# Performance work log

Measured on AMD Instinct MI355X. Metric: run time of the kernel, lower is better.

Reference implementation:

```python
import jax, jax.numpy as jnp
import numpy as np

COST_BBOX = 5.0
COST_GIOU = 2.0


def box_cxcywh_to_xyxy(b):
    cx, cy, w, h = b[:, 0], b[:, 1], b[:, 2], b[:, 3]
    return jnp.stack([cx - 0.5 * w, cy - 0.5 * h, cx + 0.5 * w, cy + 0.5 * h], axis=-1)


def generalized_box_iou(boxes1, boxes2):
    # boxes1 [N,4], boxes2 [M,4] in xyxy -> [N,M] GIoU
    area1 = (boxes1[:, 2] - boxes1[:, 0]) * (boxes1[:, 3] - boxes1[:, 1])
    area2 = (boxes2[:, 2] - boxes2[:, 0]) * (boxes2[:, 3] - boxes2[:, 1])
    lt = jnp.maximum(boxes1[:, None, :2], boxes2[None, :, :2])
    rb = jnp.minimum(boxes1[:, None, 2:], boxes2[None, :, 2:])
    wh = jnp.clip(rb - lt, 0.0)
    inter = wh[..., 0] * wh[..., 1]
    union = area1[:, None] + area2[None, :] - inter
    iou = inter / union
    lt_e = jnp.minimum(boxes1[:, None, :2], boxes2[None, :, :2])
    rb_e = jnp.maximum(boxes1[:, None, 2:], boxes2[None, :, 2:])
    wh_e = jnp.clip(rb_e - lt_e, 0.0)
    area_e = wh_e[..., 0] * wh_e[..., 1]
    return iou - (area_e - union) / area_e


@jax.jit
def cost_matrix(pred_boxes, truth_boxes):
    B, Q, _ = pred_boxes.shape
    out_bbox = pred_boxes.reshape(-1, 4)   # [B*Q,4]
    tgt_bbox = truth_boxes.reshape(-1, 4)  # [B*T,4]
    cost_bbox = jnp.sum(jnp.abs(out_bbox[:, None, :] - tgt_bbox[None, :, :]), axis=-1)  # L1 cdist
    cost_giou = -generalized_box_iou(box_cxcywh_to_xyxy(out_bbox), box_cxcywh_to_xyxy(tgt_bbox))
    C = COST_BBOX * cost_bbox + COST_GIOU * cost_giou
    return C.reshape(B, Q, -1)


def _lsa_rows_le_cols(cost):
    # Jonker-Volgenant shortest augmenting path (same algorithm as scipy
    # linear_sum_assignment). cost: [R, C] float64 with R <= C.
    # Returns col4row: assigned column for each row.
    R, Cc = cost.shape
    u = np.zeros(R)
    v = np.zeros(Cc)
    col4row = np.full(R, -1, dtype=np.int64)
    row4col = np.full(Cc, -1, dtype=np.int64)
    for cur in range(R):
        shortest = np.full(Cc, np.inf)
        path = np.full(Cc, -1, dtype=np.int64)
        on_row = np.zeros(R, dtype=bool)
        on_col = np.zeros(Cc, dtype=bool)
        min_val = 0.0
        i = cur
        sink = -1
        while sink == -1:
            on_row[i] = True
            rem = np.where(~on_col)[0]
            d = min_val + cost[i, rem] - u[i] - v[rem]
            better = d < shortest[rem]
            upd = rem[better]
            shortest[upd] = d[better]
            path[upd] = i
            j = rem[np.argmin(shortest[rem])]
            min_val = shortest[j]
            on_col[j] = True
            if row4col[j] == -1:
                sink = j
            else:
                i = row4col[j]
        u[cur] += min_val
        rset = np.where(on_row)[0]
        rset = rset[rset != cur]
        u[rset] += min_val - shortest[col4row[rset]]
        cset = np.where(on_col)[0]
        v[cset] -= min_val - shortest[cset]
        # augment along the path back from sink
        j = sink
        while True:
            i = path[j]
            row4col[j] = i
            col4row[i], j = j, col4row[i]
            if i == cur:
                break
    return col4row


def setup_inputs() -> dict:
    key = jax.random.key(0)
    k1, k2 = jax.random.split(key)
    pred_boxes = jax.random.uniform(k1, (32, 300, 4), dtype=jnp.float32)
    truth_boxes = jax.random.uniform(k2, (32, 50, 4), dtype=jnp.float32)
    return {"pred_boxes": pred_boxes, "truth_boxes": truth_boxes}


def reference(pred_boxes, truth_boxes):
    B, Q = pred_boxes.shape[:2]
    T = truth_boxes.shape[1]
    C = np.asarray(cost_matrix(pred_boxes, truth_boxes))  # [B, Q, B*T] (host, like .cpu())
    results = []
    for b in range(B):
        c = C[b, :, b * T:(b + 1) * T]  # diagonal block [Q, T]
        # Q > T: solve on the transpose (rows = targets), as scipy does internally.
        col4row = _lsa_rows_le_cols(np.ascontiguousarray(c.T, dtype=np.float64))
        i = col4row                     # selected query per target
        j = np.arange(T, dtype=np.int64)
        order = np.argsort(i)           # scipy returns row indices sorted
        results.append(np.stack([i[order], j[order]]))
    return jnp.asarray(np.stack(results), dtype=jnp.int64)  # [B, 2, min(Q,T)]
```

## Files before the change

kernel.cpp:

```cpp
#include <hip/hip_runtime.h>


#define NQ 300
#define NT 50
#define NSLOT 5
#define STRIDE 301
#define NTHREADS 256
#define ARR_CAP 4

typedef unsigned long long u64_t;

__device__ __forceinline__ u64_t minu64(u64_t a, u64_t b) { return a < b ? a : b; }

__device__ __forceinline__ u64_t f64_key(double d) {
    u64_t u = __builtin_bit_cast(u64_t, d);
    u ^= (u64_t)((long long)u >> 63) | 0x8000000000000000ull;
    return u;
}
__device__ __forceinline__ double key_f64(u64_t k) {
    u64_t u = (k >> 63) ? (k ^ 0x8000000000000000ull) : ~k;
    return __builtin_bit_cast(double, u);
}
__device__ __forceinline__ u64_t pack_key(double d, int j) {
    return (f64_key(d) & ~511ull) | (u64_t)(unsigned)j;
}

template<int CTRL, int RMASK>
__device__ __forceinline__ u64_t dpp_u64(u64_t x) {
    int lo = (int)(unsigned)(x & 0xffffffffull);
    int hi = (int)(unsigned)(x >> 32);
    int plo = __builtin_amdgcn_update_dpp(lo, lo, CTRL, RMASK, 0xf, false);
    int phi = __builtin_amdgcn_update_dpp(hi, hi, CTRL, RMASK, 0xf, false);
    return ((u64_t)(unsigned)phi << 32) | (u64_t)(unsigned)plo;
}

__device__ __forceinline__ u64_t wave_min_u64(u64_t k) {
    k = minu64(k, dpp_u64<0x121, 0xf>(k));
    k = minu64(k, dpp_u64<0x122, 0xf>(k));
    k = minu64(k, dpp_u64<0x124, 0xf>(k));
    k = minu64(k, dpp_u64<0x128, 0xf>(k));
    k = minu64(k, dpp_u64<0x142, 0xa>(k));
    k = minu64(k, dpp_u64<0x143, 0xc>(k));
    int lo = __builtin_amdgcn_readlane((int)(unsigned)(k & 0xffffffffull), 63);
    int hi = __builtin_amdgcn_readlane((int)(unsigned)(k >> 32), 63);
    return ((u64_t)(unsigned)hi << 32) | (u64_t)(unsigned)lo;
}

__device__ __forceinline__ double readlane_f64(double x, int l) {
    u64_t u = __builtin_bit_cast(u64_t, x);
    int lo = __builtin_amdgcn_readlane((int)(unsigned)(u & 0xffffffffull), l);
    int hi = __builtin_amdgcn_readlane((int)(unsigned)(u >> 32), l);
    return __builtin_bit_cast(double, ((u64_t)(unsigned)hi << 32) | (u64_t)(unsigned)lo);
}

__device__ __forceinline__ void wave_sync() { __builtin_amdgcn_wave_barrier(); }

#define SEL5(res, a, kidx) do { (res) = a[0]; \
    if ((kidx) == 1) (res) = a[1]; if ((kidx) == 2) (res) = a[2]; \
    if ((kidx) == 3) (res) = a[3]; if ((kidx) == 4) (res) = a[4]; } while (0)
#define SET5(a, kidx, val) do { \
    if ((kidx) == 0) a[0] = (val); if ((kidx) == 1) a[1] = (val); \
    if ((kidx) == 2) a[2] = (val); if ((kidx) == 3) a[3] = (val); \
    if ((kidx) == 4) a[4] = (val); } while (0)

__global__ __launch_bounds__(NTHREADS) void hungarian_kernel(
    const float* __restrict__ pred, const float* __restrict__ truth,
    int* __restrict__ out)
{
#pragma clang fp contract(off)
    const int b = blockIdx.x;
    const int tid = threadIdx.x;
    const int lane = tid & 63;
    const int wav = tid >> 6;

    __shared__ float cost[NT * STRIDE];
    __shared__ int claim[NQ];
    __shared__ double sh_short[NQ];
    __shared__ int sh_c4r[NT];

    const float* pb = pred + b * NQ * 4;
    const float* tb = truth + b * NT * 4;

    for (int idx = tid; idx < NT * NQ; idx += NTHREADS) {
        int t = idx / NQ;
        int q = idx - t * NQ;
        float pcx = pb[q*4+0], pcy = pb[q*4+1], pw = pb[q*4+2], ph = pb[q*4+3];
        float tcx = tb[t*4+0], tcy = tb[t*4+1], tw = tb[t*4+2], th = tb[t*4+3];
        float cb = ((fabsf(pcx-tcx) + fabsf(pcy-tcy)) + fabsf(pw-tw)) + fabsf(ph-th);
        float px1 = pcx - 0.5f*pw, py1 = pcy - 0.5f*ph;
        float px2 = pcx + 0.5f*pw, py2 = pcy + 0.5f*ph;
        float tx1 = tcx - 0.5f*tw, ty1 = tcy - 0.5f*th;
        float tx2 = tcx + 0.5f*tw, ty2 = tcy + 0.5f*th;
        float area1 = (px2-px1)*(py2-py1);
        float area2 = (tx2-tx1)*(ty2-ty1);
        float ltx = fmaxf(px1, tx1), lty = fmaxf(py1, ty1);
        float rbx = fminf(px2, tx2), rby = fminf(py2, ty2);
        float w = fmaxf(rbx-ltx, 0.f), h = fmaxf(rby-lty, 0.f);
        float inter = w*h;
        float uni = (area1 + area2) - inter;
        float iou = inter/uni;
        float ex1 = fminf(px1,tx1), ey1 = fminf(py1,ty1);
        float ex2 = fmaxf(px2,tx2), ey2 = fmaxf(py2,ty2);
        float ew = fmaxf(ex2-ex1, 0.f), eh = fmaxf(ey2-ey1, 0.f);
        float ae = ew*eh;
        float g = iou - (ae - uni)/ae;
        cost[t*STRIDE + q] = 5.0f*cb + 2.0f*(-g);
    }
    for (int j = tid; j < NQ; j += NTHREADS) claim[j] = 0x7fffffff;
    __syncthreads();

    float rm = __builtin_inff();
    int ram = 0;
    if (tid < NT) {
        const float* row = cost + tid * STRIDE;
        float m0 = __builtin_inff(), m1 = m0, m2 = m0, m3 = m0;
        int a0 = 0, a1 = 0, a2 = 0, a3 = 0;
        for (int c = 0; c < NQ; c += 4) {
            float x0 = row[c], x1 = row[c+1], x2 = row[c+2], x3 = row[c+3];
            if (x0 < m0) { m0 = x0; a0 = c; }
            if (x1 < m1) { m1 = x1; a1 = c+1; }
            if (x2 < m2) { m2 = x2; a2 = c+2; }
            if (x3 < m3) { m3 = x3; a3 = c+3; }
        }
        rm = m0; ram = a0;
        if (m1 < rm || (m1 == rm && a1 < ram)) { rm = m1; ram = a1; }
        if (m2 < rm || (m2 == rm && a2 < ram)) { rm = m2; ram = a2; }
        if (m3 < rm || (m3 == rm && a3 < ram)) { rm = m3; ram = a3; }
        atomicMin(&claim[ram], tid);
    }
    __syncthreads();
    if (wav != 0) return;

    double u_reg = (tid < NT) ? (double)rm : 0.0;
    int c4r = -1;
    if (tid < NT && claim[ram] == tid) c4r = ram;
    double v_reg[NSLOT];
    int r4c_reg[NSLOT];
#pragma unroll
    for (int k = 0; k < NSLOT; ++k) {
        int j = lane + (k << 6);
        v_reg[k] = 0.0;
        int cl = (j < NQ) ? claim[j] : 0x7fffffff;
        r4c_reg[k] = (cl != 0x7fffffff) ? cl : -1;
    }
    int att_cnt = 0;
    u64_t arr = __ballot(tid < NT && c4r < 0);
    u64_t dij = 0;

    while (arr) {
        int i = __builtin_ctzll(arr);
        arr &= arr - 1;
        const float* crow = cost + i * STRIDE;
        u64_t k1 = ~0ull;
        double v1 = __builtin_inf(), v2 = __builtin_inf();
#pragma unroll
        for (int k = 0; k < NSLOT; ++k) {
            int j = lane + (k << 6);
            if (j < NQ) {
                double m = (double)crow[j] - v_reg[k];
                u64_t kk = pack_key(m, j);
                if (kk < k1) { v2 = v1; v1 = m; k1 = kk; }
                else if (m < v2) { v2 = m; }
            }
        }
        u64_t kmin = wave_min_u64(k1);
        int j1 = (int)(kmin & 511ull);
        int kj = j1 >> 6, lj = j1 & 63;
        double v1g = readlane_f64(v1, lj);
        double cand = (lane == lj) ? v2 : v1;
        double v2g = key_f64(wave_min_u64(f64_key(cand)));
        int rsel; SEL5(rsel, r4c_reg, kj);
        int r = __builtin_amdgcn_readlane(rsel, lj);
        if (r < 0) {
            if (lane == lj) SET5(r4c_reg, kj, i);
            if (lane == i) { c4r = j1; u_reg = v1g; }
        } else {
            double cij = (double)crow[j1];
            if (lane == lj) { SET5(r4c_reg, kj, i); SET5(v_reg, kj, cij - v2g); }
            if (lane == i) { c4r = j1; u_reg = v2g; }
            if (lane == r) { c4r = -1; att_cnt++; }
            int ac = __builtin_amdgcn_readlane(att_cnt, r);
            u64_t rb = 1ull << r;
            if (ac <= ARR_CAP) arr |= rb; else dij |= rb;
        }
    }

    while (dij) {
        int cur = __builtin_ctzll(dij);
        dij &= dij - 1;
        unsigned oncol = 0;
        u64_t onrow = 0;
        double short_reg[NSLOT];
        int path_reg[NSLOT];
#pragma unroll
        for (int k = 0; k < NSLOT; ++k) { short_reg[k] = __builtin_inf(); path_reg[k] = -1; }
        double min_val = 0.0;
        int i = cur, sink = -1;

        while (sink < 0) {
            onrow |= 1ull << i;
            double u_i = readlane_f64(u_reg, i);
            const float* crow = cost + i * STRIDE;
            u64_t bk = ~0ull;
#pragma unroll
            for (int k = 0; k < NSLOT; ++k) {
                int j = lane + (k << 6);
                if (j < NQ && !((oncol >> k) & 1u)) {
                    double d = ((min_val + (double)crow[j]) - u_i) - v_reg[k];
                    if (d < short_reg[k]) { short_reg[k] = d; path_reg[k] = i; }
                    u64_t kk = pack_key(short_reg[k], j);
                    if (kk < bk) bk = kk;
                }
            }
            bk = wave_min_u64(bk);
            int j = (int)(bk & 511ull);
            int kj = j >> 6, lj = j & 63;
            double ssel; SEL5(ssel, short_reg, kj);
            min_val = readlane_f64(ssel, lj);
            if (lane == lj) oncol |= 1u << kj;
            int rsel; SEL5(rsel, r4c_reg, kj);
            int r = __builtin_amdgcn_readlane(rsel, lj);
            if (r < 0) sink = j; else i = r;
        }

#pragma unroll
        for (int k = 0; k < NSLOT; ++k) {
            int j = lane + (k << 6);
            if (j < NQ) sh_short[j] = short_reg[k];
        }
        wave_sync();
        double ss = (tid < NT && c4r >= 0) ? sh_short[c4r] : 0.0;
        if (tid < NT) {
            if (tid == cur) u_reg = u_reg + min_val;
            else if ((onrow >> tid) & 1ull) u_reg = u_reg + (min_val - ss);
        }
#pragma unroll
        for (int k = 0; k < NSLOT; ++k) {
            int j = lane + (k << 6);
            if (j < NQ && ((oncol >> k) & 1u))
                v_reg[k] = v_reg[k] - (min_val - short_reg[k]);
        }

        int jj = sink;
        while (true) {
            int kk2 = jj >> 6, ll = jj & 63;
            int psel; SEL5(psel, path_reg, kk2);
            int ii = __builtin_amdgcn_readlane(psel, ll);
            if (lane == ll) SET5(r4c_reg, kk2, ii);
            int nj = __builtin_amdgcn_readlane(c4r, ii);
            if (lane == ii) c4r = jj;
            jj = nj;
            if (ii == cur) break;
        }
    }

    if (tid < NT) sh_c4r[tid] = c4r;
    wave_sync();
    if (tid < NT) {
        int it = c4r;
        int rank = 0;
        for (int t2 = 0; t2 < NT; ++t2) rank += (sh_c4r[t2] < it) ? 1 : 0;
        out[b * 2 * NT + rank] = it;
        out[b * 2 * NT + NT + rank] = tid;
    }
}

extern "C" void kernel_launch(void* const* d_in, const int* in_sizes, int n_in,
                              void* d_out, int out_size, void* d_ws, size_t ws_size,
                              hipStream_t stream) {
    const float* pred  = (const float*)d_in[0];
    const float* truth = (const float*)d_in[1];
    int* out = (int*)d_out;
    hungarian_kernel<<<32, NTHREADS, 0, stream>>>(pred, truth, out);
}
```

Before: 93.95 us.

## Fuse top-two wave reduction, parallelize row minima, cache packed keys in Dijkstra

The auction phase now carries the best and second-best values through one combined DPP butterfly instead of two separate 64-bit min reductions and a readlane. The initial row-minimum scan is split across 200 threads, each covering a quarter of a row, with a small merge step afterwards. The Dijkstra inner loop keeps a cached packed key per column, so the key is rebuilt only when a shortest distance improves and visited columns are masked with an all-ones key. ARR_CAP is raised from 4 to 6 so more rows stay in the cheap auction path, and launch bounds gain a minimum-blocks hint of 1; both shift work between phases in ways that may change behavior.

```diff
diff --git a/kernel.cpp b/kernel.cpp
--- a/kernel.cpp
+++ b/kernel.cpp
@@ -6,7 +6,7 @@
 #define NSLOT 5
 #define STRIDE 301
 #define NTHREADS 256
-#define ARR_CAP 4
+#define ARR_CAP 6
 
 typedef unsigned long long u64_t;
 
@@ -16,10 +16,6 @@
     u64_t u = __builtin_bit_cast(u64_t, d);
     u ^= (u64_t)((long long)u >> 63) | 0x8000000000000000ull;
     return u;
-}
-__device__ __forceinline__ double key_f64(u64_t k) {
-    u64_t u = (k >> 63) ? (k ^ 0x8000000000000000ull) : ~k;
-    return __builtin_bit_cast(double, u);
 }
 __device__ __forceinline__ u64_t pack_key(double d, int j) {
     return (f64_key(d) & ~511ull) | (u64_t)(unsigned)j;
@@ -33,6 +29,19 @@
     int phi = __builtin_amdgcn_update_dpp(hi, hi, CTRL, RMASK, 0xf, false);
     return ((u64_t)(unsigned)phi << 32) | (u64_t)(unsigned)plo;
 }
+template<int CTRL, int RMASK>
+__device__ __forceinline__ double dpp_f64(double x) {
+    return __builtin_bit_cast(double, dpp_u64<CTRL, RMASK>(__builtin_bit_cast(u64_t, x)));
+}
+
+__device__ __forceinline__ u64_t readlane_u64(u64_t u, int l) {
+    int lo = __builtin_amdgcn_readlane((int)(unsigned)(u & 0xffffffffull), l);
+    int hi = __builtin_amdgcn_readlane((int)(unsigned)(u >> 32), l);
+    return ((u64_t)(unsigned)hi << 32) | (u64_t)(unsigned)lo;
+}
+__device__ __forceinline__ double readlane_f64(double x, int l) {
+    return __builtin_bit_cast(double, readlane_u64(__builtin_bit_cast(u64_t, x), l));
+}
 
 __device__ __forceinline__ u64_t wave_min_u64(u64_t k) {
     k = minu64(k, dpp_u64<0x121, 0xf>(k));
@@ -41,16 +50,7 @@
     k = minu64(k, dpp_u64<0x128, 0xf>(k));
     k = minu64(k, dpp_u64<0x142, 0xa>(k));
     k = minu64(k, dpp_u64<0x143, 0xc>(k));
-    int lo = __builtin_amdgcn_readlane((int)(unsigned)(k & 0xffffffffull), 63);
-    int hi = __builtin_amdgcn_readlane((int)(unsigned)(k >> 32), 63);
-    return ((u64_t)(unsigned)hi << 32) | (u64_t)(unsigned)lo;
-}
-
-__device__ __forceinline__ double readlane_f64(double x, int l) {
-    u64_t u = __builtin_bit_cast(u64_t, x);
-    int lo = __builtin_amdgcn_readlane((int)(unsigned)(u & 0xffffffffull), l);
-    int hi = __builtin_amdgcn_readlane((int)(unsigned)(u >> 32), l);
-    return __builtin_bit_cast(double, ((u64_t)(unsigned)hi << 32) | (u64_t)(unsigned)lo);
+    return readlane_u64(k, 63);
 }
 
 __device__ __forceinline__ void wave_sync() { __builtin_amdgcn_wave_barrier(); }
@@ -63,7 +63,16 @@
     if ((kidx) == 2) a[2] = (val); if ((kidx) == 3) a[3] = (val); \
     if ((kidx) == 4) a[4] = (val); } while (0)
 
-__global__ __launch_bounds__(NTHREADS) void hungarian_kernel(
+#define JSTEP(CTRL, RMASK) do { \
+    u64_t ok = dpp_u64<CTRL, RMASK>(k1); \
+    double ov1 = dpp_f64<CTRL, RMASK>(v1); \
+    double ov2 = dpp_f64<CTRL, RMASK>(v2); \
+    double lose = (ok < k1) ? v1 : ov1; \
+    v2 = fmin(fmin(v2, ov2), lose); \
+    if (ok < k1) { k1 = ok; v1 = ov1; } \
+} while (0)
+
+__global__ __launch_bounds__(NTHREADS, 1) void hungarian_kernel(
     const float* __restrict__ pred, const float* __restrict__ truth,
     int* __restrict__ out)
 {
@@ -109,23 +118,30 @@
     for (int j = tid; j < NQ; j += NTHREADS) claim[j] = 0x7fffffff;
     __syncthreads();
 
+    float* smin = (float*)sh_short;
+    int* samin = (int*)(smin + 200);
+    if (tid < 200) {
+        int row = tid % 50, seg = tid / 50;
+        int c0 = seg * 75;
+        const float* rp = cost + row * STRIDE + c0;
+        float m = __builtin_inff(); int a = 0;
+        for (int c = 0; c < 75; ++c) {
+            float x = rp[c];
+            if (x < m) { m = x; a = c0 + c; }
+        }
+        smin[seg*50 + row] = m;
+        samin[seg*50 + row] = a;
+    }
+    __syncthreads();
+
     float rm = __builtin_inff();
     int ram = 0;
     if (tid < NT) {
-        const float* row = cost + tid * STRIDE;
-        float m0 = __builtin_inff(), m1 = m0, m2 = m0, m3 = m0;
-        int a0 = 0, a1 = 0, a2 = 0, a3 = 0;
-        for (int c = 0; c < NQ; c += 4) {
-            float x0 = row[c], x1 = row[c+1], x2 = row[c+2], x3 = row[c+3];
-            if (x0 < m0) { m0 = x0; a0 = c; }
-            if (x1 < m1) { m1 = x1; a1 = c+1; }
-            if (x2 < m2) { m2 = x2; a2 = c+2; }
-            if (x3 < m3) { m3 = x3; a3 = c+3; }
-        }
-        rm = m0; ram = a0;
-        if (m1 < rm || (m1 == rm && a1 < ram)) { rm = m1; ram = a1; }
-        if (m2 < rm || (m2 == rm && a2 < ram)) { rm = m2; ram = a2; }
-        if (m3 < rm || (m3 == rm && a3 < ram)) { rm = m3; ram = a3; }
+        rm = smin[tid]; ram = samin[tid];
+        for (int s = 1; s < 4; ++s) {
+            float ms = smin[s*50 + tid]; int as = samin[s*50 + tid];
+            if (ms < rm || (ms == rm && as < ram)) { rm = ms; ram = as; }
+        }
         atomicMin(&claim[ram], tid);
     }
     __syncthreads();
@@ -160,15 +176,16 @@
                 double m = (double)crow[j] - v_reg[k];
                 u64_t kk = pack_key(m, j);
                 if (kk < k1) { v2 = v1; v1 = m; k1 = kk; }
-                else if (m < v2) { v2 = m; }
+                else v2 = fmin(v2, m);
             }
         }
-        u64_t kmin = wave_min_u64(k1);
+        JSTEP(0x121, 0xf); JSTEP(0x122, 0xf); JSTEP(0x124, 0xf); JSTEP(0x128, 0xf);
+        JSTEP(0x142, 0xa); JSTEP(0x143, 0xc);
+        u64_t kmin = readlane_u64(k1, 63);
+        double v1g = readlane_f64(v1, 63);
+        double v2g = readlane_f64(v2, 63);
         int j1 = (int)(kmin & 511ull);
         int kj = j1 >> 6, lj = j1 & 63;
-        double v1g = readlane_f64(v1, lj);
-        double cand = (lane == lj) ? v2 : v1;
-        double v2g = key_f64(wave_min_u64(f64_key(cand)));
         int rsel; SEL5(rsel, r4c_reg, kj);
         int r = __builtin_amdgcn_readlane(rsel, lj);
         if (r < 0) {
@@ -191,9 +208,12 @@
         unsigned oncol = 0;
         u64_t onrow = 0;
         double short_reg[NSLOT];
+        u64_t short_key[NSLOT];
         int path_reg[NSLOT];
 #pragma unroll
-        for (int k = 0; k < NSLOT; ++k) { short_reg[k] = __builtin_inf(); path_reg[k] = -1; }
+        for (int k = 0; k < NSLOT; ++k) {
+            short_reg[k] = __builtin_inf(); short_key[k] = ~0ull; path_reg[k] = -1;
+        }
         double min_val = 0.0;
         int i = cur, sink = -1;
 
@@ -207,17 +227,19 @@
                 int j = lane + (k << 6);
                 if (j < NQ && !((oncol >> k) & 1u)) {
                     double d = ((min_val + (double)crow[j]) - u_i) - v_reg[k];
-                    if (d < short_reg[k]) { short_reg[k] = d; path_reg[k] = i; }
-                    u64_t kk = pack_key(short_reg[k], j);
-                    if (kk < bk) bk = kk;
+                    if (d < short_reg[k]) {
+                        short_reg[k] = d; path_reg[k] = i;
+                        short_key[k] = pack_key(d, j);
+                    }
                 }
+                bk = minu64(bk, short_key[k]);
             }
             bk = wave_min_u64(bk);
             int j = (int)(bk & 511ull);
             int kj = j >> 6, lj = j & 63;
             double ssel; SEL5(ssel, short_reg, kj);
             min_val = readlane_f64(ssel, lj);
-            if (lane == lj) oncol |= 1u << kj;
+            if (lane == lj) { oncol |= 1u << kj; SET5(short_key, kj, ~0ull); }
             int rsel; SEL5(rsel, r4c_reg, kj);
             int r = __builtin_amdgcn_readlane(rsel, lj);
             if (r < 0) sink = j; else i = r;
```

Result: faster. 88.22 us (-6.1%).
